# Optimization experiments

Hardware: AMD Instinct MI355X
Metric: run time of the kernel (lower is better)

## Reference

```python
import jax, jax.numpy as jnp
import numpy as np

N, E, D, L = 50000, 800000, 128, 3  # nodes, edges, feature dim, layers
BN_EPS = 1e-5


def setup_inputs() -> dict:
    key = jax.random.key(0)
    ks = jax.random.split(key, 6)
    x = jax.random.normal(ks[0], (N, D), dtype=jnp.float32)
    edge_index = jax.random.randint(ks[1], (2, E), 0, N, dtype=jnp.int64)
    eps = jnp.zeros((L,), dtype=jnp.float32)
    # Linear weights ~ fan-in scaled init for numerical sanity
    W1 = jax.random.normal(ks[2], (L, D, D), dtype=jnp.float32) * (1.0 / np.sqrt(D))
    b1 = jnp.zeros((L, D), dtype=jnp.float32)
    W2 = jax.random.normal(ks[3], (L, D, D), dtype=jnp.float32) * (1.0 / np.sqrt(D))
    b2 = jnp.zeros((L, D), dtype=jnp.float32)
    bn1_g = jnp.ones((L, D), dtype=jnp.float32)
    bn1_b = jnp.zeros((L, D), dtype=jnp.float32)
    bn2_g = jnp.ones((L, D), dtype=jnp.float32)
    bn2_b = jnp.zeros((L, D), dtype=jnp.float32)
    return {"x": x, "edge_index": edge_index, "eps": eps, "W1": W1, "b1": b1,
            "bn1_g": bn1_g, "bn1_b": bn1_b, "W2": W2, "b2": b2,
            "bn2_g": bn2_g, "bn2_b": bn2_b}


def _batchnorm(h, g, b):
    # training-mode BatchNorm1d over node axis
    mu = h.mean(axis=0)
    var = h.var(axis=0)
    return (h - mu) * jax.lax.rsqrt(var + BN_EPS) * g + b


def reference(x, edge_index, eps, W1, b1, bn1_g, bn1_b, W2, b2, bn2_g, bn2_b):
    src = edge_index[0]
    dst = edge_index[1]
    h = x
    for l in range(L):
        # message: relu(x_j) gathered per edge; aggregate: scatter-add at dst
        agg = jax.ops.segment_sum(jax.nn.relu(h[src]), dst, num_segments=N)
        z = (1.0 + eps[l]) * h + agg
        # GINConv.mlp: Linear -> BN -> ReLU -> Linear
        z = _batchnorm(z @ W1[l] + b1[l], bn1_g[l], bn1_b[l])
        z = jax.nn.relu(z) @ W2[l] + b2[l]
        # outer per-layer BatchNorm
        z = _batchnorm(z, bn2_g[l], bn2_b[l])
        # ReLU on all but last layer (dropout is identity in eval)
        h = jax.nn.relu(z) if l < L - 1 else z
    return h
```

## Files before the change

### kernel.cpp

```cpp
#include <hip/hip_runtime.h>

#define N_NODES 50000
#define DIM 128
#define BN_EPS 1e-5f

__global__ __launch_bounds__(256) void edge_hist(const int* __restrict__ dst,
                                                 int* __restrict__ cnt, int E) {
  const int e = blockIdx.x * blockDim.x + threadIdx.x;
  if (e < E) atomicAdd(&cnt[dst[e]], 1);
}

__global__ __launch_bounds__(1024) void edge_scan(const int* __restrict__ cnt,
                                                  int* __restrict__ row_ptr) {
  __shared__ int part[1024];
  const int tid = threadIdx.x;
  const int per = (N_NODES + 1023) / 1024;
  const int start = tid * per;
  const int end = min(start + per, N_NODES);
  int s = 0;
  for (int i = start; i < end; ++i) s += cnt[i];
  part[tid] = s;
  __syncthreads();
  for (int off = 1; off < 1024; off <<= 1) {
    const int v = part[tid];
    const int u = (tid >= off) ? part[tid - off] : 0;
    __syncthreads();
    part[tid] = v + u;
    __syncthreads();
  }
  int run = (tid == 0) ? 0 : part[tid - 1];
  for (int i = start; i < end; ++i) {
    row_ptr[i] = run;
    run += cnt[i];
  }
  if (tid == 1023) row_ptr[N_NODES] = run;
}

__global__ __launch_bounds__(256) void edge_fill(const int* __restrict__ src,
                                                 const int* __restrict__ dst,
                                                 const int* __restrict__ row_ptr,
                                                 int* __restrict__ cur,
                                                 int* __restrict__ srcl, int E) {
  const int e = blockIdx.x * blockDim.x + threadIdx.x;
  if (e < E) {
    const int d = dst[e];
    const int pos = row_ptr[d] + atomicAdd(&cur[d], 1);
    srcl[pos] = src[e];
  }
}

__global__ __launch_bounds__(256) void aggregate_combine(
    const float* __restrict__ h, const int* __restrict__ row_ptr,
    const int* __restrict__ srcl, const float* __restrict__ eps_l,
    float* __restrict__ z) {
  const int node = (blockIdx.x * blockDim.x + threadIdx.x) >> 6;
  const int lane = threadIdx.x & 63;
  if (node >= N_NODES) return;
  const float epsv = 1.0f + *eps_l;
  const size_t col = (size_t)lane * 2;
  float2 acc;
  {
    const float2 hv = *reinterpret_cast<const float2*>(h + (size_t)node * DIM + col);
    acc.x = epsv * hv.x;
    acc.y = epsv * hv.y;
  }
  int p = row_ptr[node];
  const int pe = row_ptr[node + 1];
  for (; p + 4 <= pe; p += 4) {
    const int s0 = srcl[p + 0], s1 = srcl[p + 1];
    const int s2 = srcl[p + 2], s3 = srcl[p + 3];
    const float2 v0 = *reinterpret_cast<const float2*>(h + (size_t)s0 * DIM + col);
    const float2 v1 = *reinterpret_cast<const float2*>(h + (size_t)s1 * DIM + col);
    const float2 v2 = *reinterpret_cast<const float2*>(h + (size_t)s2 * DIM + col);
    const float2 v3 = *reinterpret_cast<const float2*>(h + (size_t)s3 * DIM + col);
    acc.x += fmaxf(v0.x, 0.f) + fmaxf(v1.x, 0.f) + fmaxf(v2.x, 0.f) + fmaxf(v3.x, 0.f);
    acc.y += fmaxf(v0.y, 0.f) + fmaxf(v1.y, 0.f) + fmaxf(v2.y, 0.f) + fmaxf(v3.y, 0.f);
  }
  for (; p < pe; ++p) {
    const int s = srcl[p];
    const float2 v = *reinterpret_cast<const float2*>(h + (size_t)s * DIM + col);
    acc.x += fmaxf(v.x, 0.f);
    acc.y += fmaxf(v.y, 0.f);
  }
  *reinterpret_cast<float2*>(z + (size_t)node * DIM + col) = acc;
}

template <int MODE>
__global__ __launch_bounds__(256) void gemm_bn(
    const float* __restrict__ in0,
    const float* __restrict__ ac,
    const float* __restrict__ W,
    const float* __restrict__ bias,
    float* __restrict__ out,
    float* __restrict__ stats) {
  __shared__ float w_lds[32][DIM];
  __shared__ float z_lds[64][32];

  const int tid = threadIdx.x;
  const int group = tid >> 5;
  const int lane = tid & 31;
  const int row0 = blockIdx.x * 64;

  float4 acc[8];
#pragma unroll
  for (int r = 0; r < 8; ++r) acc[r] = make_float4(0.f, 0.f, 0.f, 0.f);

  for (int kc = 0; kc < 4; ++kc) {
    const int kbase = kc * 32;
#pragma unroll
    for (int it = 0; it < 4; ++it) {
      const int krow = (tid >> 5) + it * 8;
      const int j4 = (tid & 31) * 4;
      *reinterpret_cast<float4*>(&w_lds[krow][j4]) =
          *reinterpret_cast<const float4*>(&W[(size_t)(kbase + krow) * DIM + j4]);
    }
#pragma unroll
    for (int it = 0; it < 2; ++it) {
      const int rl = (tid >> 3) + it * 32;
      const int kk4 = (tid & 7) * 4;
      const int rowg = row0 + rl;
      float4 z = make_float4(0.f, 0.f, 0.f, 0.f);
      if (rowg < N_NODES) {
        const size_t off = (size_t)rowg * DIM + kbase + kk4;
        const float4 tv = *reinterpret_cast<const float4*>(&in0[off]);
        if (MODE == 1) {
          const float4 aa = *reinterpret_cast<const float4*>(&ac[kbase + kk4]);
          const float4 cc = *reinterpret_cast<const float4*>(&ac[DIM + kbase + kk4]);
          z.x = fmaxf(aa.x * tv.x + cc.x, 0.f);
          z.y = fmaxf(aa.y * tv.y + cc.y, 0.f);
          z.z = fmaxf(aa.z * tv.z + cc.z, 0.f);
          z.w = fmaxf(aa.w * tv.w + cc.w, 0.f);
        } else {
          z = tv;
        }
      }
      *reinterpret_cast<float4*>(&z_lds[rl][kk4]) = z;
    }
    __syncthreads();
#pragma unroll
    for (int k = 0; k < 32; k += 4) {
      const float4 w0 = *reinterpret_cast<const float4*>(&w_lds[k + 0][lane * 4]);
      const float4 w1 = *reinterpret_cast<const float4*>(&w_lds[k + 1][lane * 4]);
      const float4 w2 = *reinterpret_cast<const float4*>(&w_lds[k + 2][lane * 4]);
      const float4 w3 = *reinterpret_cast<const float4*>(&w_lds[k + 3][lane * 4]);
#pragma unroll
      for (int r = 0; r < 8; ++r) {
        const float4 z4 =
            *reinterpret_cast<const float4*>(&z_lds[group * 8 + r][k]);
        acc[r].x += z4.x * w0.x + z4.y * w1.x + z4.z * w2.x + z4.w * w3.x;
        acc[r].y += z4.x * w0.y + z4.y * w1.y + z4.z * w2.y + z4.w * w3.y;
        acc[r].z += z4.x * w0.z + z4.y * w1.z + z4.z * w2.z + z4.w * w3.z;
        acc[r].w += z4.x * w0.w + z4.y * w1.w + z4.z * w2.w + z4.w * w3.w;
      }
    }
    __syncthreads();
  }

  const float4 bv = *reinterpret_cast<const float4*>(&bias[lane * 4]);
  float4 s1 = make_float4(0.f, 0.f, 0.f, 0.f);
  float4 s2 = make_float4(0.f, 0.f, 0.f, 0.f);
#pragma unroll
  for (int r = 0; r < 8; ++r) {
    const int rowg = row0 + group * 8 + r;
    if (rowg < N_NODES) {
      float4 v;
      v.x = acc[r].x + bv.x;
      v.y = acc[r].y + bv.y;
      v.z = acc[r].z + bv.z;
      v.w = acc[r].w + bv.w;
      *reinterpret_cast<float4*>(&out[(size_t)rowg * DIM + lane * 4]) = v;
      s1.x += v.x; s1.y += v.y; s1.z += v.z; s1.w += v.w;
      s2.x += v.x * v.x; s2.y += v.y * v.y; s2.z += v.z * v.z; s2.w += v.w * v.w;
    }
  }
  __syncthreads();
  float* red = &w_lds[0][0];
  red[group * DIM + lane * 4 + 0] = s1.x;
  red[group * DIM + lane * 4 + 1] = s1.y;
  red[group * DIM + lane * 4 + 2] = s1.z;
  red[group * DIM + lane * 4 + 3] = s1.w;
  red[1024 + group * DIM + lane * 4 + 0] = s2.x;
  red[1024 + group * DIM + lane * 4 + 1] = s2.y;
  red[1024 + group * DIM + lane * 4 + 2] = s2.z;
  red[1024 + group * DIM + lane * 4 + 3] = s2.w;
  __syncthreads();
  if (tid < DIM) {
    float a = 0.f, b = 0.f;
#pragma unroll
    for (int g = 0; g < 8; ++g) {
      a += red[g * DIM + tid];
      b += red[1024 + g * DIM + tid];
    }
    atomicAdd(&stats[tid], a);
    atomicAdd(&stats[DIM + tid], b);
  }
}

__global__ void bn_param(const float* __restrict__ stats,
                         const float* __restrict__ g,
                         const float* __restrict__ b, float* __restrict__ ac) {
  const int j = threadIdx.x;
  const float invN = 1.0f / (float)N_NODES;
  const float mu = stats[j] * invN;
  const float var = stats[DIM + j] * invN - mu * mu;
  const float a = g[j] * rsqrtf(var + BN_EPS);
  ac[j] = a;
  ac[DIM + j] = b[j] - mu * a;
}

template <int RELU>
__global__ __launch_bounds__(256) void apply_bn(const float* __restrict__ t,
                                                const float* __restrict__ ac,
                                                float* __restrict__ out) {
  const int i = blockIdx.x * blockDim.x + threadIdx.x;
  const int k = (i * 4) & (DIM - 1);
  const float4 v = *reinterpret_cast<const float4*>(&t[(size_t)i * 4]);
  const float4 a = *reinterpret_cast<const float4*>(&ac[k]);
  const float4 c = *reinterpret_cast<const float4*>(&ac[DIM + k]);
  float4 r;
  r.x = a.x * v.x + c.x;
  r.y = a.y * v.y + c.y;
  r.z = a.z * v.z + c.z;
  r.w = a.w * v.w + c.w;
  if (RELU) {
    r.x = fmaxf(r.x, 0.f);
    r.y = fmaxf(r.y, 0.f);
    r.z = fmaxf(r.z, 0.f);
    r.w = fmaxf(r.w, 0.f);
  }
  *reinterpret_cast<float4*>(&out[(size_t)i * 4]) = r;
}

extern "C" void kernel_launch(void* const* d_in, const int* in_sizes, int n_in,
                              void* d_out, int out_size, void* d_ws,
                              size_t ws_size, hipStream_t stream) {
  const float* x = (const float*)d_in[0];
  const int* ei = (const int*)d_in[1];
  const float* eps = (const float*)d_in[2];
  const float* W1 = (const float*)d_in[3];
  const float* b1 = (const float*)d_in[4];
  const float* g1 = (const float*)d_in[5];
  const float* bb1 = (const float*)d_in[6];
  const float* W2 = (const float*)d_in[7];
  const float* b2 = (const float*)d_in[8];
  const float* g2 = (const float*)d_in[9];
  const float* bb2 = (const float*)d_in[10];

  const int E = in_sizes[1] / 2;
  const size_t ND = (size_t)N_NODES * DIM;

  float* bufZ = (float*)d_ws;
  float* bufH = bufZ + ND;
  float* stats = bufH + ND;
  float* bnp = stats + 512;
  int* cnt = (int*)(bnp + 512);
  int* row_ptr = cnt + N_NODES;
  int* cur = row_ptr + N_NODES + 1;
  int* srcl = cur + N_NODES;

  const int gemm_grid = (N_NODES + 63) / 64;
  const int apply_grid = (N_NODES * DIM / 4) / 256;
  const int edge_grid = (E + 255) / 256;
  const int agg_grid = (N_NODES * 64 + 255) / 256;

  hipMemsetAsync(cnt, 0, sizeof(int) * (size_t)N_NODES * 2 + sizeof(int),
                 stream);
  hipMemsetAsync(cur, 0, sizeof(int) * (size_t)N_NODES, stream);
  edge_hist<<<edge_grid, 256, 0, stream>>>(ei + E, cnt, E);
  edge_scan<<<1, 1024, 0, stream>>>(cnt, row_ptr);
  edge_fill<<<edge_grid, 256, 0, stream>>>(ei, ei + E, row_ptr, cur, srcl, E);

  const float* h = x;
  for (int l = 0; l < 3; ++l) {
    hipMemsetAsync(stats, 0, sizeof(float) * 512, stream);
    aggregate_combine<<<agg_grid, 256, 0, stream>>>(h, row_ptr, srcl, eps + l,
                                                    bufZ);
    gemm_bn<2><<<gemm_grid, 256, 0, stream>>>(bufZ, nullptr,
                                              W1 + (size_t)l * DIM * DIM,
                                              b1 + l * DIM, bufZ, stats);
    bn_param<<<1, DIM, 0, stream>>>(stats, g1 + l * DIM, bb1 + l * DIM, bnp);
    gemm_bn<1><<<gemm_grid, 256, 0, stream>>>(bufZ, bnp,
                                              W2 + (size_t)l * DIM * DIM,
                                              b2 + l * DIM, bufZ, stats + 256);
    bn_param<<<1, DIM, 0, stream>>>(stats + 256, g2 + l * DIM, bb2 + l * DIM,
                                    bnp + 256);
    if (l < 2) {
      apply_bn<1><<<apply_grid, 256, 0, stream>>>(bufZ, bnp + 256, bufH);
      h = bufH;
    } else {
      apply_bn<0><<<apply_grid, 256, 0, stream>>>(bufZ, bnp + 256,
                                                  (float*)d_out);
    }
  }
}
```

Before: 878.7 us.

## Fuse outer BN+ReLU into aggregation and rewrite GEMM as register-tiled row-per-lane

The per-layer BatchNorm+ReLU apply pass for the first two layers is removed. That normalization is applied on the fly inside the next layer's gather-aggregate kernel, which now also unrolls 8 neighbors per iteration. The LDS-tiled GEMM is replaced by a kernel where each lane owns one row and 32 output columns, reading weights as wave-uniform scalar loads, and the BN statistics are reduced via cross-lane shuffles. Buffers are ping-ponged so that only a final apply pass is needed. This saves two full-tensor read/write passes, but the BN affine now runs per gathered edge, and the new GEMM loses coalescing on row reads and needs many registers.

```diff
diff --git a/kernel.cpp b/kernel.cpp
--- a/kernel.cpp
+++ b/kernel.cpp
@@ -49,150 +49,187 @@
   }
 }
 
+template <int FUSE>
 __global__ __launch_bounds__(256) void aggregate_combine(
-    const float* __restrict__ h, const int* __restrict__ row_ptr,
+    const float* __restrict__ h, const int* __restrict__ rp,
     const int* __restrict__ srcl, const float* __restrict__ eps_l,
-    float* __restrict__ z) {
-  const int node = (blockIdx.x * blockDim.x + threadIdx.x) >> 6;
+    const float* __restrict__ ac, float* __restrict__ z) {
+  const int node =
+      __builtin_amdgcn_readfirstlane(blockIdx.x * 4 + (threadIdx.x >> 6));
+  if (node >= N_NODES) return;
   const int lane = threadIdx.x & 63;
-  if (node >= N_NODES) return;
+  const int col = lane * 2;
+
+  float2 av, cv;
+  if (FUSE) {
+    av.x = ac[col]; av.y = ac[col + 1];
+    cv.x = ac[DIM + col]; cv.y = ac[DIM + col + 1];
+  }
   const float epsv = 1.0f + *eps_l;
-  const size_t col = (size_t)lane * 2;
+
   float2 acc;
   {
-    const float2 hv = *reinterpret_cast<const float2*>(h + (size_t)node * DIM + col);
-    acc.x = epsv * hv.x;
-    acc.y = epsv * hv.y;
-  }
-  int p = row_ptr[node];
-  const int pe = row_ptr[node + 1];
-  for (; p + 4 <= pe; p += 4) {
-    const int s0 = srcl[p + 0], s1 = srcl[p + 1];
-    const int s2 = srcl[p + 2], s3 = srcl[p + 3];
-    const float2 v0 = *reinterpret_cast<const float2*>(h + (size_t)s0 * DIM + col);
-    const float2 v1 = *reinterpret_cast<const float2*>(h + (size_t)s1 * DIM + col);
-    const float2 v2 = *reinterpret_cast<const float2*>(h + (size_t)s2 * DIM + col);
-    const float2 v3 = *reinterpret_cast<const float2*>(h + (size_t)s3 * DIM + col);
-    acc.x += fmaxf(v0.x, 0.f) + fmaxf(v1.x, 0.f) + fmaxf(v2.x, 0.f) + fmaxf(v3.x, 0.f);
-    acc.y += fmaxf(v0.y, 0.f) + fmaxf(v1.y, 0.f) + fmaxf(v2.y, 0.f) + fmaxf(v3.y, 0.f);
+    const float2 u =
+        *reinterpret_cast<const float2*>(h + (size_t)node * DIM + col);
+    float2 s;
+    if (FUSE) {
+      s.x = fmaxf(fmaf(av.x, u.x, cv.x), 0.f);
+      s.y = fmaxf(fmaf(av.y, u.y, cv.y), 0.f);
+    } else {
+      s = u;
+    }
+    acc.x = epsv * s.x;
+    acc.y = epsv * s.y;
+  }
+
+  int p = rp[node];
+  const int pe = rp[node + 1];
+  for (; p + 8 <= pe; p += 8) {
+    int s[8];
+#pragma unroll
+    for (int i = 0; i < 8; ++i) s[i] = srcl[p + i];
+    float2 v[8];
+#pragma unroll
+    for (int i = 0; i < 8; ++i)
+      v[i] = *reinterpret_cast<const float2*>(h + (size_t)s[i] * DIM + col);
+#pragma unroll
+    for (int i = 0; i < 8; ++i) {
+      float mx, my;
+      if (FUSE) {
+        mx = fmaxf(fmaf(av.x, v[i].x, cv.x), 0.f);
+        my = fmaxf(fmaf(av.y, v[i].y, cv.y), 0.f);
+      } else {
+        mx = fmaxf(v[i].x, 0.f);
+        my = fmaxf(v[i].y, 0.f);
+      }
+      acc.x += mx;
+      acc.y += my;
+    }
   }
   for (; p < pe; ++p) {
     const int s = srcl[p];
-    const float2 v = *reinterpret_cast<const float2*>(h + (size_t)s * DIM + col);
-    acc.x += fmaxf(v.x, 0.f);
-    acc.y += fmaxf(v.y, 0.f);
+    const float2 v =
+        *reinterpret_cast<const float2*>(h + (size_t)s * DIM + col);
+    if (FUSE) {
+      acc.x += fmaxf(fmaf(av.x, v.x, cv.x), 0.f);
+      acc.y += fmaxf(fmaf(av.y, v.y, cv.y), 0.f);
+    } else {
+      acc.x += fmaxf(v.x, 0.f);
+      acc.y += fmaxf(v.y, 0.f);
+    }
   }
   *reinterpret_cast<float2*>(z + (size_t)node * DIM + col) = acc;
 }
 
 template <int MODE>
-__global__ __launch_bounds__(256) void gemm_bn(
-    const float* __restrict__ in0,
-    const float* __restrict__ ac,
-    const float* __restrict__ W,
-    const float* __restrict__ bias,
-    float* __restrict__ out,
-    float* __restrict__ stats) {
-  __shared__ float w_lds[32][DIM];
-  __shared__ float z_lds[64][32];
-
-  const int tid = threadIdx.x;
-  const int group = tid >> 5;
-  const int lane = tid & 31;
-  const int row0 = blockIdx.x * 64;
-
-  float4 acc[8];
-#pragma unroll
-  for (int r = 0; r < 8; ++r) acc[r] = make_float4(0.f, 0.f, 0.f, 0.f);
-
-  for (int kc = 0; kc < 4; ++kc) {
-    const int kbase = kc * 32;
-#pragma unroll
-    for (int it = 0; it < 4; ++it) {
-      const int krow = (tid >> 5) + it * 8;
-      const int j4 = (tid & 31) * 4;
-      *reinterpret_cast<float4*>(&w_lds[krow][j4]) =
-          *reinterpret_cast<const float4*>(&W[(size_t)(kbase + krow) * DIM + j4]);
+__global__ __launch_bounds__(256) void gemm_rw(
+    const float* __restrict__ in, const float* __restrict__ ac,
+    const float* __restrict__ W, const float* __restrict__ bias,
+    float* __restrict__ out, float* __restrict__ stats) {
+  const int lane = threadIdx.x & 63;
+  const int colb = __builtin_amdgcn_readfirstlane((threadIdx.x >> 6) * 32);
+  const int row = blockIdx.x * 64 + lane;
+  const bool valid = row < N_NODES;
+  const float* __restrict__ zr = in + (size_t)(valid ? row : 0) * DIM;
+
+  float acc[32];
+#pragma unroll
+  for (int j = 0; j < 32; ++j) acc[j] = 0.f;
+
+#define LDCH(Z0, Z1, CH)                                                    \
+  {                                                                         \
+    const int kb_ = (CH) * 8;                                               \
+    Z0 = *reinterpret_cast<const float4*>(zr + kb_);                        \
+    Z1 = *reinterpret_cast<const float4*>(zr + kb_ + 4);                    \
+    if (MODE == 1) {                                                        \
+      const float4 A0_ = *reinterpret_cast<const float4*>(ac + kb_);        \
+      const float4 A1_ = *reinterpret_cast<const float4*>(ac + kb_ + 4);    \
+      const float4 C0_ = *reinterpret_cast<const float4*>(ac + DIM + kb_);  \
+      const float4 C1_ = *reinterpret_cast<const float4*>(ac + DIM + kb_ + 4); \
+      Z0.x = fmaxf(fmaf(A0_.x, Z0.x, C0_.x), 0.f);                          \
+      Z0.y = fmaxf(fmaf(A0_.y, Z0.y, C0_.y), 0.f);                          \
+      Z0.z = fmaxf(fmaf(A0_.z, Z0.z, C0_.z), 0.f);                          \
+      Z0.w = fmaxf(fmaf(A0_.w, Z0.w, C0_.w), 0.f);                          \
+      Z1.x = fmaxf(fmaf(A1_.x, Z1.x, C1_.x), 0.f);                          \
+      Z1.y = fmaxf(fmaf(A1_.y, Z1.y, C1_.y), 0.f);                          \
+      Z1.z = fmaxf(fmaf(A1_.z, Z1.z, C1_.z), 0.f);                          \
+      Z1.w = fmaxf(fmaf(A1_.w, Z1.w, C1_.w), 0.f);                          \
+    }                                                                       \
+  }
+
+#define FMAK(ZK, KG)                                                        \
+  {                                                                         \
+    const float* __restrict__ wk_ = W + (size_t)(KG)*DIM + colb;            \
+    _Pragma("unroll") for (int j = 0; j < 32; ++j) acc[j] =                 \
+        fmaf(wk_[j], (ZK), acc[j]);                                         \
+  }
+
+#define FMACH(Z0, Z1, CH)                                                   \
+  {                                                                         \
+    const int kb0_ = (CH) * 8;                                              \
+    FMAK(Z0.x, kb0_ + 0) FMAK(Z0.y, kb0_ + 1)                               \
+    FMAK(Z0.z, kb0_ + 2) FMAK(Z0.w, kb0_ + 3)                               \
+    FMAK(Z1.x, kb0_ + 4) FMAK(Z1.y, kb0_ + 5)                               \
+    FMAK(Z1.z, kb0_ + 6) FMAK(Z1.w, kb0_ + 7)                               \
+  }
+
+  float4 a0, a1, b0, b1;
+  LDCH(a0, a1, 0)
+#pragma unroll 1
+  for (int c = 0; c < 16; c += 2) {
+    LDCH(b0, b1, c + 1)
+    FMACH(a0, a1, c)
+    if (c + 2 < 16) LDCH(a0, a1, c + 2)
+    FMACH(b0, b1, c + 1)
+  }
+#undef LDCH
+#undef FMAK
+#undef FMACH
+
+  const float* __restrict__ bb = bias + colb;
+  float v[32];
+#pragma unroll
+  for (int j = 0; j < 32; ++j) v[j] = valid ? (acc[j] + bb[j]) : 0.f;
+  if (valid) {
+    float* op = out + (size_t)row * DIM + colb;
+#pragma unroll
+    for (int j4 = 0; j4 < 8; ++j4) {
+      float4 o;
+      o.x = v[j4 * 4 + 0]; o.y = v[j4 * 4 + 1];
+      o.z = v[j4 * 4 + 2]; o.w = v[j4 * 4 + 3];
+      *reinterpret_cast<float4*>(op + j4 * 4) = o;
     }
-#pragma unroll
-    for (int it = 0; it < 2; ++it) {
-      const int rl = (tid >> 3) + it * 32;
-      const int kk4 = (tid & 7) * 4;
-      const int rowg = row0 + rl;
-      float4 z = make_float4(0.f, 0.f, 0.f, 0.f);
-      if (rowg < N_NODES) {
-        const size_t off = (size_t)rowg * DIM + kbase + kk4;
-        const float4 tv = *reinterpret_cast<const float4*>(&in0[off]);
-        if (MODE == 1) {
-          const float4 aa = *reinterpret_cast<const float4*>(&ac[kbase + kk4]);
-          const float4 cc = *reinterpret_cast<const float4*>(&ac[DIM + kbase + kk4]);
-          z.x = fmaxf(aa.x * tv.x + cc.x, 0.f);
-          z.y = fmaxf(aa.y * tv.y + cc.y, 0.f);
-          z.z = fmaxf(aa.z * tv.z + cc.z, 0.f);
-          z.w = fmaxf(aa.w * tv.w + cc.w, 0.f);
-        } else {
-          z = tv;
-        }
-      }
-      *reinterpret_cast<float4*>(&z_lds[rl][kk4]) = z;
-    }
-    __syncthreads();
-#pragma unroll
-    for (int k = 0; k < 32; k += 4) {
-      const float4 w0 = *reinterpret_cast<const float4*>(&w_lds[k + 0][lane * 4]);
-      const float4 w1 = *reinterpret_cast<const float4*>(&w_lds[k + 1][lane * 4]);
-      const float4 w2 = *reinterpret_cast<const float4*>(&w_lds[k + 2][lane * 4]);
-      const float4 w3 = *reinterpret_cast<const float4*>(&w_lds[k + 3][lane * 4]);
-#pragma unroll
-      for (int r = 0; r < 8; ++r) {
-        const float4 z4 =
-            *reinterpret_cast<const float4*>(&z_lds[group * 8 + r][k]);
-        acc[r].x += z4.x * w0.x + z4.y * w1.x + z4.z * w2.x + z4.w * w3.x;
-        acc[r].y += z4.x * w0.y + z4.y * w1.y + z4.z * w2.y + z4.w * w3.y;
-        acc[r].z += z4.x * w0.z + z4.y * w1.z + z4.z * w2.z + z4.w * w3.z;
-        acc[r].w += z4.x * w0.w + z4.y * w1.w + z4.z * w2.w + z4.w * w3.w;
-      }
-    }
-    __syncthreads();
-  }
-
-  const float4 bv = *reinterpret_cast<const float4*>(&bias[lane * 4]);
-  float4 s1 = make_float4(0.f, 0.f, 0.f, 0.f);
-  float4 s2 = make_float4(0.f, 0.f, 0.f, 0.f);
-#pragma unroll
-  for (int r = 0; r < 8; ++r) {
-    const int rowg = row0 + group * 8 + r;
-    if (rowg < N_NODES) {
-      float4 v;
-      v.x = acc[r].x + bv.x;
-      v.y = acc[r].y + bv.y;
-      v.z = acc[r].z + bv.z;
-      v.w = acc[r].w + bv.w;
-      *reinterpret_cast<float4*>(&out[(size_t)rowg * DIM + lane * 4]) = v;
-      s1.x += v.x; s1.y += v.y; s1.z += v.z; s1.w += v.w;
-      s2.x += v.x * v.x; s2.y += v.y * v.y; s2.z += v.z * v.z; s2.w += v.w * v.w;
-    }
-  }
-  __syncthreads();
-  float* red = &w_lds[0][0];
-  red[group * DIM + lane * 4 + 0] = s1.x;
-  red[group * DIM + lane * 4 + 1] = s1.y;
-  red[group * DIM + lane * 4 + 2] = s1.z;
-  red[group * DIM + lane * 4 + 3] = s1.w;
-  red[1024 + group * DIM + lane * 4 + 0] = s2.x;
-  red[1024 + group * DIM + lane * 4 + 1] = s2.y;
-  red[1024 + group * DIM + lane * 4 + 2] = s2.z;
-  red[1024 + group * DIM + lane * 4 + 3] = s2.w;
-  __syncthreads();
-  if (tid < DIM) {
-    float a = 0.f, b = 0.f;
-#pragma unroll
-    for (int g = 0; g < 8; ++g) {
-      a += red[g * DIM + tid];
-      b += red[1024 + g * DIM + tid];
-    }
-    atomicAdd(&stats[tid], a);
-    atomicAdd(&stats[DIM + tid], b);
+  }
+  float q[16];
+#pragma unroll
+  for (int jj = 0; jj < 16; ++jj) {
+    const bool hi = (lane & 32) != 0;
+    const float keep = hi ? v[jj + 16] : v[jj];
+    const float send = hi ? v[jj] : v[jj + 16];
+    const float recv = __shfl_xor(send, 32);
+    v[jj] = keep + recv;
+    q[jj] = keep * keep + recv * recv;
+  }
+#define RSTEP(ARR, CNT, O)                                                  \
+  {                                                                         \
+    _Pragma("unroll") for (int jj = 0; jj < (CNT); ++jj) {                  \
+      const bool hi_ = (lane & (O)) != 0;                                   \
+      const float keep_ = hi_ ? ARR[jj + (CNT)] : ARR[jj];                  \
+      const float send_ = hi_ ? ARR[jj] : ARR[jj + (CNT)];                  \
+      ARR[jj] = keep_ + __shfl_xor(send_, (O));                             \
+    }                                                                       \
+  }
+  RSTEP(v, 8, 16) RSTEP(q, 8, 16)
+  RSTEP(v, 4, 8)  RSTEP(q, 4, 8)
+  RSTEP(v, 2, 4)  RSTEP(q, 2, 4)
+  RSTEP(v, 1, 2)  RSTEP(q, 1, 2)
+#undef RSTEP
+  v[0] += __shfl_xor(v[0], 1);
+  q[0] += __shfl_xor(q[0], 1);
+  if ((lane & 1) == 0) {
+    const int jc = colb + (lane >> 1);
+    atomicAdd(&stats[jc], v[0]);
+    atomicAdd(&stats[DIM + jc], q[0]);
   }
 }
 
@@ -208,7 +245,6 @@
   ac[DIM + j] = b[j] - mu * a;
 }
 
-template <int RELU>
 __global__ __launch_bounds__(256) void apply_bn(const float* __restrict__ t,
                                                 const float* __restrict__ ac,
                                                 float* __restrict__ out) {
@@ -218,16 +254,10 @@
   const float4 a = *reinterpret_cast<const float4*>(&ac[k]);
   const float4 c = *reinterpret_cast<const float4*>(&ac[DIM + k]);
   float4 r;
-  r.x = a.x * v.x + c.x;
-  r.y = a.y * v.y + c.y;
-  r.z = a.z * v.z + c.z;
-  r.w = a.w * v.w + c.w;
-  if (RELU) {
-    r.x = fmaxf(r.x, 0.f);
-    r.y = fmaxf(r.y, 0.f);
-    r.z = fmaxf(r.z, 0.f);
-    r.w = fmaxf(r.w, 0.f);
-  }
+  r.x = fmaf(a.x, v.x, c.x);
+  r.y = fmaf(a.y, v.y, c.y);
+  r.z = fmaf(a.z, v.z, c.z);
+  r.w = fmaf(a.w, v.w, c.w);
   *reinterpret_cast<float4*>(&out[(size_t)i * 4]) = r;
 }
 
@@ -249,47 +279,48 @@
   const int E = in_sizes[1] / 2;
   const size_t ND = (size_t)N_NODES * DIM;
 
-  float* bufZ = (float*)d_ws;
-  float* bufH = bufZ + ND;
-  float* stats = bufH + ND;
+  float* bufA = (float*)d_ws;
+  float* bufB = bufA + ND;
+  float* stats = bufB + ND;
   float* bnp = stats + 512;
   int* cnt = (int*)(bnp + 512);
   int* row_ptr = cnt + N_NODES;
   int* cur = row_ptr + N_NODES + 1;
   int* srcl = cur + N_NODES;
 
+  const int edge_grid = (E + 255) / 256;
+  const int agg_grid = (N_NODES + 3) / 4;
   const int gemm_grid = (N_NODES + 63) / 64;
   const int apply_grid = (N_NODES * DIM / 4) / 256;
-  const int edge_grid = (E + 255) / 256;
-  const int agg_grid = (N_NODES * 64 + 255) / 256;
-
-  hipMemsetAsync(cnt, 0, sizeof(int) * (size_t)N_NODES * 2 + sizeof(int),
-                 stream);
+
+  hipMemsetAsync(cnt, 0, sizeof(int) * (size_t)N_NODES, stream);
   hipMemsetAsync(cur, 0, sizeof(int) * (size_t)N_NODES, stream);
   edge_hist<<<edge_grid, 256, 0, stream>>>(ei + E, cnt, E);
   edge_scan<<<1, 1024, 0, stream>>>(cnt, row_ptr);
   edge_fill<<<edge_grid, 256, 0, stream>>>(ei, ei + E, row_ptr, cur, srcl, E);
 
-  const float* h = x;
+  const float* hin = x;
+  float* zb = bufA;
+  float* tb = bufB;
   for (int l = 0; l < 3; ++l) {
     hipMemsetAsync(stats, 0, sizeof(float) * 512, stream);
-    aggregate_combine<<<agg_grid, 256, 0, stream>>>(h, row_ptr, srcl, eps + l,
-                                                    bufZ);
-    gemm_bn<2><<<gemm_grid, 256, 0, stream>>>(bufZ, nullptr,
-                                              W1 + (size_t)l * DIM * DIM,
-                                              b1 + l * DIM, bufZ, stats);
+    if (l == 0)
+      aggregate_combine<0><<<agg_grid, 256, 0, stream>>>(hin, row_ptr, srcl,
+                                                         eps + l, nullptr, zb);
+    else
+      aggregate_combine<1><<<agg_grid, 256, 0, stream>>>(
+          hin, row_ptr, srcl, eps + l, bnp + 256, zb);
+    gemm_rw<2><<<gemm_grid, 256, 0, stream>>>(
+        zb, nullptr, W1 + (size_t)l * DIM * DIM, b1 + l * DIM, tb, stats);
     bn_param<<<1, DIM, 0, stream>>>(stats, g1 + l * DIM, bb1 + l * DIM, bnp);
-    gemm_bn<1><<<gemm_grid, 256, 0, stream>>>(bufZ, bnp,
-                                              W2 + (size_t)l * DIM * DIM,
-                                              b2 + l * DIM, bufZ, stats + 256);
+    gemm_rw<1><<<gemm_grid, 256, 0, stream>>>(
+        tb, bnp, W2 + (size_t)l * DIM * DIM, b2 + l * DIM, zb, stats + 256);
     bn_param<<<1, DIM, 0, stream>>>(stats + 256, g2 + l * DIM, bb2 + l * DIM,
                                     bnp + 256);
-    if (l < 2) {
-      apply_bn<1><<<apply_grid, 256, 0, stream>>>(bufZ, bnp + 256, bufH);
-      h = bufH;
-    } else {
-      apply_bn<0><<<apply_grid, 256, 0, stream>>>(bufZ, bnp + 256,
-                                                  (float*)d_out);
-    }
-  }
-}
+    hin = zb;
+    float* tmp = zb;
+    zb = tb;
+    tb = tmp;
+  }
+  apply_bn<<<apply_grid, 256, 0, stream>>>(hin, bnp + 256, (float*)d_out);
+}
```

Measured after the change: 883.7 us. About the same (+0.6%).
